# Kernel optimization log

Hardware: AMD Instinct MI355X
Metric: run time of the kernel (lower is better)

## Reference

```python
import math
import jax, jax.numpy as jnp
import numpy as np

WIDTH = 512
F_TOT = 1024          # min(2*width, 2048)
F_CHUNK = 128
RHO = 0.25
SPECTRAL_SCALE = 0.8
ES_BETA = 6.0
TAU = 0.001
EPS = 1e-8
LN_EPS = 1e-5
N_TOKENS = 4096


def setup_inputs() -> dict:
    key = jax.random.key(0)
    ks = jax.random.split(key, 4)
    x = jax.random.normal(ks[0], (N_TOKENS, WIDTH), dtype=jnp.float32)
    # freq init: linspace(-pi, pi, F) repeated across width
    freq = jnp.tile(jnp.linspace(-math.pi, math.pi, F_TOT, dtype=jnp.float32)[:, None], (1, WIDTH))
    alpha = jax.random.normal(ks[1], (F_TOT, WIDTH), dtype=jnp.float32) * 0.01
    gate = jnp.ones((F_TOT, WIDTH), dtype=jnp.float32) * 0.01
    ln_gamma = jnp.ones((WIDTH,), dtype=jnp.float32)
    ln_beta = jnp.zeros((WIDTH,), dtype=jnp.float32)
    # torch Linear default init: U(-1/sqrt(in), 1/sqrt(in))
    bound = 1.0 / math.sqrt(WIDTH)
    w_loc = jax.random.uniform(ks[2], (WIDTH, WIDTH), dtype=jnp.float32, minval=-bound, maxval=bound)
    b_loc = jax.random.uniform(ks[3], (WIDTH,), dtype=jnp.float32, minval=-bound, maxval=bound)
    return {"x": x, "freq": freq, "alpha": alpha, "gate": gate,
            "ln_gamma": ln_gamma, "ln_beta": ln_beta, "w_loc": w_loc, "b_loc": b_loc}


def reference(x, freq, alpha, gate, ln_gamma, ln_beta, w_loc, b_loc):
    # LayerNorm
    mu = jnp.mean(x, axis=-1, keepdims=True)
    var = jnp.mean((x - mu) ** 2, axis=-1, keepdims=True)
    x_n = (x - mu) / jnp.sqrt(var + LN_EPS) * ln_gamma + ln_beta

    # local branch: Linear -> GELU (exact erf, torch default)
    h_local = jax.nn.gelu(x_n @ w_loc.T + b_loc, approximate=False)

    # spectral weights
    f = freq * SPECTRAL_SCALE
    denom = jax.lax.stop_gradient(jnp.max(jnp.abs(f)))  # .detach().abs().amax()
    safe = jnp.where(denom < 1e-8, 1.0, denom)
    win = jnp.where(denom < 1e-8, jnp.ones_like(f), jnp.exp(-ES_BETA * (f / safe) ** 2))
    raw = alpha * gate
    thr_w = jnp.sign(raw) * jax.nn.relu(jnp.abs(raw) - TAU) * win

    # chunked sin basis expansion, accumulated with lax.scan
    n_chunks = F_TOT // F_CHUNK
    f_r = f.reshape(n_chunks, F_CHUNK, WIDTH)
    t_r = thr_w.reshape(n_chunks, F_CHUNK, WIDTH)

    def body(acc, ft):
        fc, tc = ft  # [C, W] each
        basis = jnp.sin(x_n[:, None, :] * fc[None, :, :])  # [N, C, W]
        return acc + jnp.einsum('ncw,cw->nw', basis, tc), None

    h_spec, _ = jax.lax.scan(jax.checkpoint(body), jnp.zeros_like(x_n), (f_r, t_r))

    # RMS normalize over width
    rms = jnp.sqrt(jnp.mean(h_spec ** 2, axis=1, keepdims=True) + EPS)
    h_spec = h_spec / rms
    return h_local + RHO * h_spec
```

## Files before the change

### kernel.cpp

```cpp
#include <hip/hip_runtime.h>
#include <hip/hip_bf16.h>
#include <math.h>

#define N_TOK 4096
#define W 512
#define F_TOT 1024
#define FW (F_TOT * W)

#define OFF_PARTIAL 0
#define OFF_NNZ     4096
#define OFF_XN      8192
#define OFF_WB      4202496
#define OFF_E       4726784
#define OFF_T       6823936
#define OFF_C       8921088

typedef __attribute__((ext_vector_type(8))) short bf16x8;
typedef __attribute__((ext_vector_type(4))) short bf16x4;
typedef __attribute__((ext_vector_type(4))) float f32x4;

__global__ __launch_bounds__(256) void ln_prep(
    const float* __restrict__ x, const float* __restrict__ freq,
    const float* __restrict__ gamma, const float* __restrict__ beta,
    const float* __restrict__ wloc, __hip_bfloat16* __restrict__ xn,
    __hip_bfloat16* __restrict__ wb, float* __restrict__ partial,
    unsigned* __restrict__ nnz) {
  const int b = blockIdx.x, t = threadIdx.x;
  const int wv = t >> 6, lane = t & 63;
  if (b < 1024) {
    const int row = b * 4 + wv;
    const float4* xr = (const float4*)(x + row * W);
    const float4 p0 = xr[lane * 2];
    const float4 p1 = xr[lane * 2 + 1];
    float s  = p0.x + p0.y + p0.z + p0.w + p1.x + p1.y + p1.z + p1.w;
    float ss = p0.x*p0.x + p0.y*p0.y + p0.z*p0.z + p0.w*p0.w
             + p1.x*p1.x + p1.y*p1.y + p1.z*p1.z + p1.w*p1.w;
#pragma unroll
    for (int m = 32; m > 0; m >>= 1) {
      s  += __shfl_xor(s, m);
      ss += __shfl_xor(ss, m);
    }
    const float mu = s * (1.0f / W);
    const float var = ss * (1.0f / W) - mu * mu;
    const float rstd = rsqrtf(var + 1e-5f);
    const float4 g0 = ((const float4*)gamma)[lane * 2];
    const float4 g1 = ((const float4*)gamma)[lane * 2 + 1];
    const float4 be0 = ((const float4*)beta)[lane * 2];
    const float4 be1 = ((const float4*)beta)[lane * 2 + 1];
    alignas(16) __hip_bfloat16 o[8];
    o[0] = __float2bfloat16((p0.x - mu) * rstd * g0.x + be0.x);
    o[1] = __float2bfloat16((p0.y - mu) * rstd * g0.y + be0.y);
    o[2] = __float2bfloat16((p0.z - mu) * rstd * g0.z + be0.z);
    o[3] = __float2bfloat16((p0.w - mu) * rstd * g0.w + be0.w);
    o[4] = __float2bfloat16((p1.x - mu) * rstd * g1.x + be1.x);
    o[5] = __float2bfloat16((p1.y - mu) * rstd * g1.y + be1.y);
    o[6] = __float2bfloat16((p1.z - mu) * rstd * g1.z + be1.z);
    o[7] = __float2bfloat16((p1.w - mu) * rstd * g1.w + be1.w);
    *(bf16x8*)(xn + row * W + lane * 8) = *(const bf16x8*)o;
  } else if (b < 1280) {
    const int b2 = b - 1024;
    const float4* fp = (const float4*)(freq + b2 * 2048 + wv * 512);
    const float4 q0 = fp[lane * 2];
    const float4 q1 = fp[lane * 2 + 1];
    float mx = fmaxf(fmaxf(fmaxf(fabsf(q0.x), fabsf(q0.y)), fmaxf(fabsf(q0.z), fabsf(q0.w))),
                     fmaxf(fmaxf(fabsf(q1.x), fabsf(q1.y)), fmaxf(fabsf(q1.z), fabsf(q1.w))));
#pragma unroll
    for (int m = 32; m > 0; m >>= 1) mx = fmaxf(mx, __shfl_xor(mx, m));
    if (lane == 0) partial[b2 * 4 + wv] = mx;
    if (b == 1024 && t == 0) *nnz = 0u;
  } else {
    const int i4 = ((b - 1280) * 256 + t);
    const float4 v = ((const float4*)wloc)[i4];
    alignas(8) __hip_bfloat16 o[4];
    o[0] = __float2bfloat16(v.x);
    o[1] = __float2bfloat16(v.y);
    o[2] = __float2bfloat16(v.z);
    o[3] = __float2bfloat16(v.w);
    *(bf16x4*)(wb + i4 * 4) = *(const bf16x4*)o;
  }
}

__global__ __launch_bounds__(256) void thr_compact(
    const float* __restrict__ freq, const float* __restrict__ alpha,
    const float* __restrict__ gate, const float* __restrict__ partial,
    unsigned* __restrict__ nnz, unsigned* __restrict__ eArr,
    float* __restrict__ tArr, float* __restrict__ cArr) {
  __shared__ float red[256];
  const int t = threadIdx.x;
  red[t] = fmaxf(fmaxf(partial[t], partial[t + 256]),
                 fmaxf(partial[t + 512], partial[t + 768]));
  __syncthreads();
  for (int s = 128; s > 0; s >>= 1) {
    if (t < s) red[t] = fmaxf(red[t], red[t + s]);
    __syncthreads();
  }
  const float denom = red[0] * 0.8f;
  const bool tiny = denom < 1e-8f;
  const float inv = tiny ? 0.0f : (1.0f / denom);
  const int base = blockIdx.x * 1024 + t;
#pragma unroll
  for (int j = 0; j < 4; ++j) {
    const int e = base + j * 256;
    const float f = freq[e] * 0.8f;
    const float raw = alpha[e] * gate[e];
    const float v = fabsf(raw) - 1e-3f;
    if (v > 0.0f) {
      const float r = f * inv;
      const float win = tiny ? 1.0f : expf(-6.0f * r * r);
      const float tw = copysignf(v, raw) * win;
      const unsigned idx = atomicAdd(nnz, 1u);
      eArr[idx] = (unsigned)e;
      tArr[idx] = tw;
      cArr[idx] = f;
    }
  }
}

__global__ __launch_bounds__(64) void gemm_gelu(
    const __hip_bfloat16* __restrict__ xn, const __hip_bfloat16* __restrict__ wb,
    const float* __restrict__ bias, float* __restrict__ out) {
  const int tm = blockIdx.x >> 3;
  const int tn = blockIdx.x & 7;
  const int lane = threadIdx.x;
  const int m = lane & 15;
  const int q = lane >> 4;
  const short* A = (const short*)xn + (tm * 16 + m) * W + q * 8;
  const short* B = (const short*)wb + (tn * 64 + m) * W + q * 8;
  f32x4 acc[4] = {};

  bf16x8 a_cur = *(const bf16x8*)A;
  bf16x8 b_cur[4];
#pragma unroll
  for (int j = 0; j < 4; ++j) b_cur[j] = *(const bf16x8*)(B + (j * 16) * W);

#pragma unroll
  for (int k0 = 0; k0 < W; k0 += 32) {
    bf16x8 a_nxt;
    bf16x8 b_nxt[4];
    if (k0 + 32 < W) {
      a_nxt = *(const bf16x8*)(A + k0 + 32);
#pragma unroll
      for (int j = 0; j < 4; ++j)
        b_nxt[j] = *(const bf16x8*)(B + (j * 16) * W + k0 + 32);
    }
#pragma unroll
    for (int j = 0; j < 4; ++j)
      acc[j] = __builtin_amdgcn_mfma_f32_16x16x32_bf16(a_cur, b_cur[j], acc[j], 0, 0, 0);
    a_cur = a_nxt;
#pragma unroll
    for (int j = 0; j < 4; ++j) b_cur[j] = b_nxt[j];
  }

#pragma unroll
  for (int j = 0; j < 4; ++j) {
    const int col = tn * 64 + j * 16 + m;
    const float bv = bias[col];
#pragma unroll
    for (int r = 0; r < 4; ++r) {
      const int row = tm * 16 + q * 4 + r;
      const float v = acc[j][r] + bv;
      const float g = 0.5f * v * (1.0f + erff(v * 0.70710678118654752f));
      out[row * W + col] = g;
    }
  }
}

__global__ __launch_bounds__(256) void spectral_final(
    const __hip_bfloat16* __restrict__ xn, const unsigned* __restrict__ nnz,
    const unsigned* __restrict__ eArr, const float* __restrict__ tArr,
    const float* __restrict__ cArr, float* __restrict__ out) {
  const unsigned cnt = *nnz;
  if (cnt == 0) return;
  __shared__ float red[256];
  const int t = threadIdx.x;
  for (int n = blockIdx.x; n < N_TOK; n += gridDim.x) {
    const int c0 = t, c1 = t + 256;
    const float x0 = __bfloat162float(xn[n * W + c0]);
    const float x1 = __bfloat162float(xn[n * W + c1]);
    float h0 = 0.0f, h1 = 0.0f;
    for (unsigned i = 0; i < cnt; ++i) {
      const unsigned e = eArr[i];
      const int we = (int)(e & (W - 1));
      const float tw = tArr[i];
      const float cf = cArr[i];
      if (we == c0) h0 += tw * sinf(x0 * cf);
      else if (we == c1) h1 += tw * sinf(x1 * cf);
    }
    red[t] = h0 * h0 + h1 * h1;
    __syncthreads();
    for (int s = 128; s > 0; s >>= 1) {
      if (t < s) red[t] += red[t + s];
      __syncthreads();
    }
    const float rms = sqrtf(red[0] * (1.0f / W) + 1e-8f);
    const float sc = 0.25f / rms;
    out[n * W + c0] += sc * h0;
    out[n * W + c1] += sc * h1;
    __syncthreads();
  }
}

extern "C" void kernel_launch(void* const* d_in, const int* in_sizes, int n_in,
                              void* d_out, int out_size, void* d_ws, size_t ws_size,
                              hipStream_t stream) {
  const float* x     = (const float*)d_in[0];
  const float* freq  = (const float*)d_in[1];
  const float* alpha = (const float*)d_in[2];
  const float* gate  = (const float*)d_in[3];
  const float* gamma = (const float*)d_in[4];
  const float* beta  = (const float*)d_in[5];
  const float* wloc  = (const float*)d_in[6];
  const float* bloc  = (const float*)d_in[7];
  float* out = (float*)d_out;

  char* ws = (char*)d_ws;
  float* partial       = (float*)(ws + OFF_PARTIAL);
  unsigned* nnz        = (unsigned*)(ws + OFF_NNZ);
  __hip_bfloat16* xn   = (__hip_bfloat16*)(ws + OFF_XN);
  __hip_bfloat16* wb   = (__hip_bfloat16*)(ws + OFF_WB);
  unsigned* eArr       = (unsigned*)(ws + OFF_E);
  float* tArr          = (float*)(ws + OFF_T);
  float* cArr          = (float*)(ws + OFF_C);

  hipLaunchKernelGGL(ln_prep, dim3(1536), dim3(256), 0, stream,
                     x, freq, gamma, beta, wloc, xn, wb, partial, nnz);
  hipLaunchKernelGGL(thr_compact, dim3(512), dim3(256), 0, stream,
                     freq, alpha, gate, partial, nnz, eArr, tArr, cArr);
  hipLaunchKernelGGL(gemm_gelu, dim3(2048), dim3(64), 0, stream,
                     xn, wb, bloc, out);
  hipLaunchKernelGGL(spectral_final, dim3(512), dim3(256), 0, stream,
                     xn, nnz, eArr, tArr, cArr, out);
}
```

Measured before the change: 103.0 us.

## Merge threshold compaction into GEMM launch and shrink spectral kernel to one wave

The threshold/compaction work now runs in the first 512 blocks of the GEMM launch (one 64-thread wave each, reducing the partial maxima via shuffles), which removes one kernel launch and lets both jobs overlap. The spectral pass now uses one wave per token with eight columns per lane and a shuffle reduction instead of an LDS tree with barriers. The price is fewer threads per compaction block, each doing more serial work, and a different lane-to-column mapping in the sparse loop.

```diff
diff --git a/kernel.cpp b/kernel.cpp
--- a/kernel.cpp
+++ b/kernel.cpp
@@ -80,48 +80,48 @@
   }
 }
 
-__global__ __launch_bounds__(256) void thr_compact(
+__global__ __launch_bounds__(64) void gemm_thr(
+    const __hip_bfloat16* __restrict__ xn, const __hip_bfloat16* __restrict__ wb,
+    const float* __restrict__ bias, float* __restrict__ out,
     const float* __restrict__ freq, const float* __restrict__ alpha,
     const float* __restrict__ gate, const float* __restrict__ partial,
     unsigned* __restrict__ nnz, unsigned* __restrict__ eArr,
     float* __restrict__ tArr, float* __restrict__ cArr) {
-  __shared__ float red[256];
-  const int t = threadIdx.x;
-  red[t] = fmaxf(fmaxf(partial[t], partial[t + 256]),
-                 fmaxf(partial[t + 512], partial[t + 768]));
-  __syncthreads();
-  for (int s = 128; s > 0; s >>= 1) {
-    if (t < s) red[t] = fmaxf(red[t], red[t + s]);
-    __syncthreads();
-  }
-  const float denom = red[0] * 0.8f;
-  const bool tiny = denom < 1e-8f;
-  const float inv = tiny ? 0.0f : (1.0f / denom);
-  const int base = blockIdx.x * 1024 + t;
-#pragma unroll
-  for (int j = 0; j < 4; ++j) {
-    const int e = base + j * 256;
-    const float f = freq[e] * 0.8f;
-    const float raw = alpha[e] * gate[e];
-    const float v = fabsf(raw) - 1e-3f;
-    if (v > 0.0f) {
-      const float r = f * inv;
-      const float win = tiny ? 1.0f : expf(-6.0f * r * r);
-      const float tw = copysignf(v, raw) * win;
-      const unsigned idx = atomicAdd(nnz, 1u);
-      eArr[idx] = (unsigned)e;
-      tArr[idx] = tw;
-      cArr[idx] = f;
-    }
-  }
-}
-
-__global__ __launch_bounds__(64) void gemm_gelu(
-    const __hip_bfloat16* __restrict__ xn, const __hip_bfloat16* __restrict__ wb,
-    const float* __restrict__ bias, float* __restrict__ out) {
-  const int tm = blockIdx.x >> 3;
-  const int tn = blockIdx.x & 7;
+  const int bid = blockIdx.x;
   const int lane = threadIdx.x;
+
+  if (bid < 512) {
+    float mx = 0.0f;
+#pragma unroll
+    for (int j = 0; j < 16; ++j) mx = fmaxf(mx, partial[lane + j * 64]);
+#pragma unroll
+    for (int m = 32; m > 0; m >>= 1) mx = fmaxf(mx, __shfl_xor(mx, m));
+    const float denom = mx * 0.8f;
+    const bool tiny = denom < 1e-8f;
+    const float inv = tiny ? 0.0f : (1.0f / denom);
+    const int base = bid * 1024 + lane;
+#pragma unroll
+    for (int j = 0; j < 16; ++j) {
+      const int e = base + j * 64;
+      const float f = freq[e] * 0.8f;
+      const float raw = alpha[e] * gate[e];
+      const float v = fabsf(raw) - 1e-3f;
+      if (v > 0.0f) {
+        const float r = f * inv;
+        const float win = tiny ? 1.0f : expf(-6.0f * r * r);
+        const float tw = copysignf(v, raw) * win;
+        const unsigned idx = atomicAdd(nnz, 1u);
+        eArr[idx] = (unsigned)e;
+        tArr[idx] = tw;
+        cArr[idx] = f;
+      }
+    }
+    return;
+  }
+
+  const int bid2 = bid - 512;
+  const int tm = bid2 >> 3;
+  const int tn = bid2 & 7;
   const int m = lane & 15;
   const int q = lane >> 4;
   const short* A = (const short*)xn + (tm * 16 + m) * W + q * 8;
@@ -165,38 +165,37 @@
   }
 }
 
-__global__ __launch_bounds__(256) void spectral_final(
+__global__ __launch_bounds__(64) void spectral_final(
     const __hip_bfloat16* __restrict__ xn, const unsigned* __restrict__ nnz,
     const unsigned* __restrict__ eArr, const float* __restrict__ tArr,
     const float* __restrict__ cArr, float* __restrict__ out) {
   const unsigned cnt = *nnz;
   if (cnt == 0) return;
-  __shared__ float red[256];
-  const int t = threadIdx.x;
+  const int lane = threadIdx.x;
   for (int n = blockIdx.x; n < N_TOK; n += gridDim.x) {
-    const int c0 = t, c1 = t + 256;
-    const float x0 = __bfloat162float(xn[n * W + c0]);
-    const float x1 = __bfloat162float(xn[n * W + c1]);
-    float h0 = 0.0f, h1 = 0.0f;
+    float xv[8], h[8];
+#pragma unroll
+    for (int j = 0; j < 8; ++j) {
+      xv[j] = __bfloat162float(xn[n * W + lane + j * 64]);
+      h[j] = 0.0f;
+    }
     for (unsigned i = 0; i < cnt; ++i) {
       const unsigned e = eArr[i];
       const int we = (int)(e & (W - 1));
-      const float tw = tArr[i];
-      const float cf = cArr[i];
-      if (we == c0) h0 += tw * sinf(x0 * cf);
-      else if (we == c1) h1 += tw * sinf(x1 * cf);
-    }
-    red[t] = h0 * h0 + h1 * h1;
-    __syncthreads();
-    for (int s = 128; s > 0; s >>= 1) {
-      if (t < s) red[t] += red[t + s];
-      __syncthreads();
-    }
-    const float rms = sqrtf(red[0] * (1.0f / W) + 1e-8f);
+      if ((we & 63) == lane) {
+        const int j = we >> 6;
+        h[j] += tArr[i] * sinf(xv[j] * cArr[i]);
+      }
+    }
+    float ss = 0.0f;
+#pragma unroll
+    for (int j = 0; j < 8; ++j) ss += h[j] * h[j];
+#pragma unroll
+    for (int m = 32; m > 0; m >>= 1) ss += __shfl_xor(ss, m);
+    const float rms = sqrtf(ss * (1.0f / W) + 1e-8f);
     const float sc = 0.25f / rms;
-    out[n * W + c0] += sc * h0;
-    out[n * W + c1] += sc * h1;
-    __syncthreads();
+#pragma unroll
+    for (int j = 0; j < 8; ++j) out[n * W + lane + j * 64] += sc * h[j];
   }
 }
 
@@ -224,10 +223,9 @@
 
   hipLaunchKernelGGL(ln_prep, dim3(1536), dim3(256), 0, stream,
                      x, freq, gamma, beta, wloc, xn, wb, partial, nnz);
-  hipLaunchKernelGGL(thr_compact, dim3(512), dim3(256), 0, stream,
-                     freq, alpha, gate, partial, nnz, eArr, tArr, cArr);
-  hipLaunchKernelGGL(gemm_gelu, dim3(2048), dim3(64), 0, stream,
-                     xn, wb, bloc, out);
-  hipLaunchKernelGGL(spectral_final, dim3(512), dim3(256), 0, stream,
+  hipLaunchKernelGGL(gemm_thr, dim3(2560), dim3(64), 0, stream,
+                     xn, wb, bloc, out, freq, alpha, gate, partial,
+                     nnz, eArr, tArr, cArr);
+  hipLaunchKernelGGL(spectral_final, dim3(512), dim3(64), 0, stream,
                      xn, nnz, eArr, tArr, cArr, out);
 }
```

Measured after the change: 100.3 us. 1.03x faster.
